# Kernel tuning notes

Measured on AMD Instinct MI355X. Metric: run time of the kernel, lower is better.

## Reference

```python
import jax, jax.numpy as jnp
import numpy as np
import math

B, S, D = 2, 2048, 2048
H = 16
DK = D // H


def build_rotary(dim, seq_len):
    inv_freq = 1.0 / (10000.0 ** (np.arange(0, dim, 2, dtype=np.float32) / dim))
    t = np.arange(seq_len, dtype=np.float32)
    freqs = np.einsum('i,j->ij', t, inv_freq)
    emb = np.concatenate([freqs, freqs], axis=-1)  # [S, dim]
    return jnp.asarray(np.cos(emb))[None, None], jnp.asarray(np.sin(emb))[None, None]


def rotate_half(x):
    x1, x2 = jnp.split(x, 2, axis=-1)
    return jnp.concatenate([-x2, x1], axis=-1)


def setup_inputs() -> dict:
    key = jax.random.key(0)
    ks = jax.random.split(key, 12)
    s = 1.0 / math.sqrt(D)
    inp = {
        'query': jax.random.normal(ks[0], (B, S, D), jnp.float32),
        'key': jax.random.normal(ks[1], (B, S, D), jnp.float32),
        'value': jax.random.normal(ks[2], (B, S, D), jnp.float32),
        'mask': jnp.tril(jnp.ones((S, S), bool))[None, None],  # causal [1,1,S,S]
        'wq': jax.random.uniform(ks[3], (D, D), jnp.float32, -s, s),
        'bq': jax.random.uniform(ks[4], (D,), jnp.float32, -s, s),
        'wk': jax.random.uniform(ks[5], (D, D), jnp.float32, -s, s),
        'bk': jax.random.uniform(ks[6], (D,), jnp.float32, -s, s),
        'wv': jax.random.uniform(ks[7], (D, D), jnp.float32, -s, s),
        'bv': jax.random.uniform(ks[8], (D,), jnp.float32, -s, s),
        'wo': jax.random.uniform(ks[9], (D, D), jnp.float32, -s, s),
        'bo': jax.random.uniform(ks[10], (D,), jnp.float32, -s, s),
    }
    return inp


def reference(query, key, value, mask, wq, bq, wk, bk, wv, bv, wo, bo):
    Bc, Sc, _ = query.shape
    # QKV projections -> [B, H, S, DK]
    def proj(x, w, b):
        return (x @ w.T + b).reshape(Bc, Sc, H, DK).transpose(0, 2, 1, 3)
    q = proj(query, wq, bq)
    k = proj(key, wk, bk)
    v = proj(value, wv, bv)
    # inline RoPE
    cos, sin = build_rotary(DK, Sc)
    cos = cos.astype(query.dtype)
    sin = sin.astype(query.dtype)
    q = q * cos + rotate_half(q) * sin
    k = k * cos + rotate_half(k) * sin
    # attention (dropout in eval / identity)
    scores = jnp.einsum('bhqd,bhkd->bhqk', q, k) / math.sqrt(DK)
    scores = jnp.where(mask, scores.astype(jnp.float32), -1e9)
    p = jax.nn.softmax(scores, axis=-1)
    x = jnp.einsum('bhqk,bhkd->bhqd', p, v)
    x = x.transpose(0, 2, 1, 3).reshape(Bc, Sc, H * DK)
    return x @ wo.T + bo
```

## Files before the change

### kernel.cpp

```cpp
#include <hip/hip_runtime.h>
#include <hip/hip_bf16.h>

#define Bc 2
#define Sc 2048
#define Dc 2048
#define Hc 16
#define DKc 128
#define Mc (Bc * Sc)
#define Kc Dc
#define Nc Dc
#define NX ((size_t)Bc * Sc * Dc)
#define NW ((size_t)Dc * Dc)

#define SM_C 0.1275174366f

typedef unsigned short u16;
using bf16x8  = __bf16 __attribute__((ext_vector_type(8)));
using ushort8 = unsigned short __attribute__((ext_vector_type(8)));
using ushort4v = unsigned short __attribute__((ext_vector_type(4)));
using floatx4 = float __attribute__((ext_vector_type(4)));
using float4v = float __attribute__((ext_vector_type(4)));

__device__ __forceinline__ u16 f2bf(float f) {
  union { float f; unsigned u; } x; x.f = f;
  unsigned r = x.u + 0x7fffu + ((x.u >> 16) & 1u);
  return (u16)(r >> 16);
}
__device__ __forceinline__ float bf2f(u16 u) {
  union { unsigned u; float f; } x; x.u = ((unsigned)u) << 16;
  return x.f;
}
__device__ __forceinline__ bf16x8 load8(const u16* p) {
  return __builtin_bit_cast(bf16x8, *(const ushort8*)p);
}
__device__ __forceinline__ floatx4 mfma16(bf16x8 a, bf16x8 b, floatx4 c) {
  return __builtin_amdgcn_mfma_f32_16x16x32_bf16(a, b, c, 0, 0, 0);
}
__device__ __forceinline__ void async16(const void* g, void* l) {
  __builtin_amdgcn_global_load_lds(
      (__attribute__((address_space(1))) void*)(g),
      (__attribute__((address_space(3))) void*)(l), 16, 0, 0);
}

__global__ __launch_bounds__(256) void cast_all(
    const float* __restrict__ q, const float* __restrict__ k,
    const float* __restrict__ v, const float* __restrict__ wq,
    const float* __restrict__ wk, const float* __restrict__ wv,
    const float* __restrict__ wo, u16* __restrict__ dst) {
  size_t i4 = (size_t)blockIdx.x * 256 + threadIdx.x;
  size_t e = i4 * 4;
  const float* src; size_t off;
  if (e < 3 * NX) {
    size_t w = e / NX;
    src = (w == 0) ? q : (w == 1) ? k : v;
    off = e - w * NX;
  } else {
    size_t e2 = e - 3 * NX;
    size_t w = e2 / NW;
    src = (w == 0) ? wq : (w == 1) ? wk : (w == 2) ? wv : wo;
    off = e2 - w * NW;
  }
  float4v val = *(const float4v*)(src + off);
  ushort4v o;
  o.x = f2bf(val.x); o.y = f2bf(val.y); o.z = f2bf(val.z); o.w = f2bf(val.w);
  *(ushort4v*)(dst + e) = o;
}

__device__ __forceinline__ void gemm_body(
    const u16* __restrict__ A, const u16* __restrict__ W,
    const float* __restrict__ bias, u16* __restrict__ out_bf,
    float* __restrict__ out_f, int epi, int m0, int n0, u16* Asl, u16* Bsl) {
  const int tid = threadIdx.x;
  const int wid = tid >> 6, lane = tid & 63;
  const int l15 = lane & 15, quad = lane >> 4;
  const int wm = wid & 1, wn = wid >> 1;

  floatx4 acc[4][4] = {};
  const int row_s = tid >> 2;
  const int col_s = (tid & 3) * 8;

  for (int k0 = 0; k0 < Kc; k0 += 32) {
    __syncthreads();
    const u16* ga0 = A + (size_t)(m0 + row_s) * Kc + k0 + col_s;
    const u16* gb0 = W + (size_t)(n0 + row_s) * Kc + k0 + col_s;
    async16(ga0, &Asl[tid * 8]);
    async16(ga0 + (size_t)64 * Kc, &Asl[2048 + tid * 8]);
    async16(gb0, &Bsl[tid * 8]);
    async16(gb0 + (size_t)64 * Kc, &Bsl[2048 + tid * 8]);
    __syncthreads();
    bf16x8 af[4], bfr[4];
#pragma unroll
    for (int i = 0; i < 4; i++)
      af[i] = load8(&Asl[(wm * 64 + i * 16 + l15) * 32 + quad * 8]);
#pragma unroll
    for (int j = 0; j < 4; j++)
      bfr[j] = load8(&Bsl[(wn * 64 + j * 16 + l15) * 32 + quad * 8]);
#pragma unroll
    for (int i = 0; i < 4; i++)
#pragma unroll
      for (int j = 0; j < 4; j++)
        acc[i][j] = mfma16(af[i], bfr[j], acc[i][j]);
  }

#pragma unroll
  for (int j = 0; j < 4; j++) {
    int col = n0 + wn * 64 + j * 16 + l15;
    float bv = bias[col];
#pragma unroll
    for (int i = 0; i < 4; i++) {
      int rowb = m0 + wm * 64 + i * 16 + quad * 4;
#pragma unroll
      for (int r = 0; r < 4; r++) {
        float v = acc[i][j][r] + bv;
        int row = rowb + r;
        if (epi == 2) {
          out_f[(size_t)row * Nc + col] = v;
        } else {
          int b = row >> 11, s = row & 2047;
          int h = col >> 7, dk = col & 127;
          size_t addr = (epi == 0)
              ? ((size_t)(b * Hc + h) * Sc + s) * DKc + dk
              : ((size_t)(b * Hc + h) * DKc + dk) * Sc + s;
          out_bf[addr] = f2bf(v);
        }
      }
    }
  }
}

__global__ __launch_bounds__(256, 2) void gemm_qkv(
    const u16* __restrict__ xq, const u16* __restrict__ xk,
    const u16* __restrict__ xv, const u16* __restrict__ wcat,
    const float* __restrict__ bq, const float* __restrict__ bk,
    const float* __restrict__ bv, u16* __restrict__ qhw,
    u16* __restrict__ khw, u16* __restrict__ vtw) {
  __shared__ u16 Asl[128 * 32];
  __shared__ u16 Bsl[128 * 32];
  const int proj = blockIdx.x >> 4;
  const int n0 = (blockIdx.x & 15) * 128;
  const int m0 = blockIdx.y * 128;
  const u16* A = (proj == 0) ? xq : (proj == 1) ? xk : xv;
  const u16* W = wcat + (size_t)proj * 2048 * Kc;
  const float* bias = (proj == 0) ? bq : (proj == 1) ? bk : bv;
  u16* outp = (proj == 0) ? qhw : (proj == 1) ? khw : vtw;
  gemm_body(A, W, bias, outp, nullptr, (proj == 2) ? 1 : 0, m0, n0, Asl, Bsl);
}

__global__ __launch_bounds__(256, 2) void gemm_out(
    const u16* __restrict__ A, const u16* __restrict__ W,
    const float* __restrict__ bias, float* __restrict__ out_f) {
  __shared__ u16 Asl[128 * 32];
  __shared__ u16 Bsl[128 * 32];
  gemm_body(A, W, bias, nullptr, out_f, 2, blockIdx.y * 128, blockIdx.x * 128,
            Asl, Bsl);
}

__global__ __launch_bounds__(256) void rope_kernel(u16* __restrict__ q,
                                                   u16* __restrict__ k) {
  int i = blockIdx.x * 256 + threadIdx.x;
  int d = i & 63;
  int s = (i >> 6) & (Sc - 1);
  int bh = i >> 17;
  size_t base = ((size_t)bh * Sc + s) * DKc;
  float inv_freq = exp2f((float)d * (-13.287712379549449f / 64.0f));
  float ang = (float)s * inv_freq;
  float sn, cs;
  sincosf(ang, &sn, &cs);
  float q1 = bf2f(q[base + d]), q2 = bf2f(q[base + d + 64]);
  q[base + d]      = f2bf((q1 * cs - q2 * sn) * SM_C);
  q[base + d + 64] = f2bf((q2 * cs + q1 * sn) * SM_C);
  float k1 = bf2f(k[base + d]), k2 = bf2f(k[base + d + 64]);
  k[base + d]      = f2bf(k1 * cs - k2 * sn);
  k[base + d + 64] = f2bf(k2 * cs + k1 * sn);
}

__global__ __launch_bounds__(256) void attn_kernel(
    const u16* __restrict__ qh, const u16* __restrict__ kh,
    const u16* __restrict__ vt, u16* __restrict__ ao) {
  __shared__ u16 Ksl[128 * 128];
  __shared__ u16 Vsl[144 * 128];
  const int tid = threadIdx.x;
  const int wid = tid >> 6, lane = tid & 63;
  const int l15 = lane & 15, quad = lane >> 4;
  const int qt = (blockIdx.z == 0) ? 15 - (int)blockIdx.x : (int)blockIdx.x;
  const int h = blockIdx.y, bb = blockIdx.z;
  const int bh = bb * Hc + h;
  const int q0 = qt * 128;
  const u16* qbase = qh + (size_t)bh * Sc * DKc;
  const u16* kbase = kh + (size_t)bh * Sc * DKc;
  const u16* vbase = vt + (size_t)bh * DKc * Sc;

  const int srow = tid >> 4;
  const int scol = (tid & 15) * 8;
  const int sdst = ((tid & 15) ^ srow) * 8;

  {
    int r = 128 + srow;
    u16 val = (r == 128) ? (u16)0x3F80 : (u16)0;
#pragma unroll
    for (int j = 0; j < 8; j++) Vsl[r * 128 + scol + j] = val;
  }

  bf16x8 qf[2][4];
#pragma unroll
  for (int mt = 0; mt < 2; mt++)
#pragma unroll
    for (int kq = 0; kq < 4; kq++)
      qf[mt][kq] = load8(qbase + (size_t)(q0 + wid * 32 + mt * 16 + l15) * DKc +
                         kq * 32 + quad * 8);

  floatx4 accO[2][9] = {};

  ushort8 kr[8], vr[8];
#pragma unroll
  for (int c = 0; c < 8; c++) {
    int rr = c * 16 + srow;
    kr[c] = *(const ushort8*)(kbase + (size_t)rr * DKc + scol);
    vr[c] = *(const ushort8*)(vbase + (size_t)rr * Sc + scol);
  }

  for (int kt = 0; kt <= qt; kt++) {
    __syncthreads();
#pragma unroll
    for (int c = 0; c < 8; c++) {
      int rr = c * 16 + srow;
      *(ushort8*)&Ksl[rr * 128 + sdst] = kr[c];
      *(ushort8*)&Vsl[rr * 128 + sdst] = vr[c];
    }
    __syncthreads();

    floatx4 sacc[2][8] = {};
#pragma unroll
    for (int kk = 0; kk < 4; kk++) {
      const int sb = ((kk * 4 + quad) ^ l15) * 8;
#pragma unroll
      for (int nt = 0; nt < 8; nt++) {
        bf16x8 kf = load8(&Ksl[(nt * 16 + l15) * 128 + sb]);
        sacc[0][nt] = mfma16(qf[0][kk], kf, sacc[0][nt]);
        sacc[1][nt] = mfma16(qf[1][kk], kf, sacc[1][nt]);
      }
    }

    if (kt == qt) {
#pragma unroll
      for (int nt = 0; nt < 8; nt++) {
        int kcol = nt * 16 + l15;
#pragma unroll
        for (int mt = 0; mt < 2; mt++) {
          int qrow = wid * 32 + mt * 16 + quad * 4;
#pragma unroll
          for (int r = 0; r < 4; r++)
            if (kcol > qrow + r) sacc[mt][nt][r] = -1e30f;
        }
      }
    }

#pragma unroll
    for (int mt = 0; mt < 2; mt++)
#pragma unroll
      for (int nt = 0; nt < 8; nt++)
#pragma unroll
        for (int r = 0; r < 4; r++)
          sacc[mt][nt][r] = exp2f(sacc[mt][nt][r]);

    __syncthreads();

    u16* Pw = &Ksl[wid * 4096];
#pragma unroll
    for (int mt = 0; mt < 2; mt++)
#pragma unroll
      for (int nt = 0; nt < 8; nt++)
#pragma unroll
        for (int r = 0; r < 4; r++) {
          int row = mt * 16 + quad * 4 + r;
          int col = nt * 16 + l15;
          int sb = (col >> 3) ^ (row & 15);
          Pw[row * 128 + sb * 8 + (col & 7)] = f2bf(sacc[mt][nt][r]);
        }

    if (kt < qt) {
      const u16* kb = kbase + (size_t)(kt + 1) * 128 * DKc;
#pragma unroll
      for (int c = 0; c < 8; c++) {
        int rr = c * 16 + srow;
        kr[c] = *(const ushort8*)(kb + (size_t)rr * DKc + scol);
        vr[c] = *(const ushort8*)(vbase + (size_t)rr * Sc + (kt + 1) * 128 + scol);
      }
    }

#pragma unroll
    for (int kk = 0; kk < 4; kk++) {
      const int sb = ((kk * 4 + quad) ^ l15) * 8;
      bf16x8 pf0 = load8(&Pw[(0 * 16 + l15) * 128 + sb]);
      bf16x8 pf1 = load8(&Pw[(1 * 16 + l15) * 128 + sb]);
#pragma unroll
      for (int nt = 0; nt < 9; nt++) {
        bf16x8 vf = load8(&Vsl[(nt * 16 + l15) * 128 + sb]);
        accO[0][nt] = mfma16(pf0, vf, accO[0][nt]);
        accO[1][nt] = mfma16(pf1, vf, accO[1][nt]);
      }
    }
  }

#pragma unroll
  for (int mt = 0; mt < 2; mt++)
#pragma unroll
    for (int r = 0; r < 4; r++) {
      float lsum = __shfl(accO[mt][8][r], lane & 48);
      float inv = 1.0f / lsum;
      int gq = q0 + wid * 32 + mt * 16 + quad * 4 + r;
      size_t rowbase = ((size_t)bb * Sc + gq) * Dc + h * DKc;
#pragma unroll
      for (int nt = 0; nt < 8; nt++)
        ao[rowbase + nt * 16 + l15] = f2bf(accO[mt][nt][r] * inv);
    }
}

extern "C" void kernel_launch(void* const* d_in, const int* in_sizes, int n_in,
                              void* d_out, int out_size, void* d_ws,
                              size_t ws_size, hipStream_t stream) {
  const float* q  = (const float*)d_in[0];
  const float* k  = (const float*)d_in[1];
  const float* v  = (const float*)d_in[2];
  const float* wq = (const float*)d_in[4];
  const float* bq = (const float*)d_in[5];
  const float* wk = (const float*)d_in[6];
  const float* bk = (const float*)d_in[7];
  const float* wv = (const float*)d_in[8];
  const float* bv = (const float*)d_in[9];
  const float* wo = (const float*)d_in[10];
  const float* bo = (const float*)d_in[11];
  float* out = (float*)d_out;

  u16* ws = (u16*)d_ws;
  u16* xq  = ws;
  u16* xk  = ws + NX;
  u16* xv  = ws + 2 * NX;
  u16* wcat = ws + 3 * NX;
  u16* wob = ws + 3 * NX + 3 * NW;
  u16* qhw = ws + 3 * NX + 4 * NW;
  u16* khw = ws + 4 * NX + 4 * NW;
  u16* vtw = ws + 5 * NX + 4 * NW;
  u16* aow = ws + 6 * NX + 4 * NW;

  {
    size_t tot4 = (3 * NX + 4 * NW) / 4;
    cast_all<<<dim3((unsigned)(tot4 / 256)), 256, 0, stream>>>(
        q, k, v, wq, wk, wv, wo, ws);
  }
  gemm_qkv<<<dim3(48, Mc / 128), 256, 0, stream>>>(
      xq, xk, xv, wcat, bq, bk, bv, qhw, khw, vtw);
  rope_kernel<<<dim3(Bc * Hc * Sc * 64 / 256), 256, 0, stream>>>(qhw, khw);
  attn_kernel<<<dim3(Sc / 128, Hc, Bc), 256, 0, stream>>>(qhw, khw, vtw, aow);
  gemm_out<<<dim3(Nc / 128, Mc / 128), 256, 0, stream>>>(aow, wob, bo, out);
}
```

Before: 534.3 us.

## Fuse Q RoPE into attention, skip masked diagonal tiles, raise GEMM occupancy

Q's rotary embedding and softmax scaling now run inside the attention kernel on register-held Q fragments, so the separate pass only rotates K. That removes one global read/write round trip over Q. On the diagonal tile, MFMAs and exp2 for fully masked 16-wide column blocks are skipped. The row-sum ones column is built in registers instead of extra LDS rows. GEMM launch bounds rise to 4 blocks per CU, which may force register spilling.

```diff
diff --git a/kernel.cpp b/kernel.cpp
--- a/kernel.cpp
+++ b/kernel.cpp
@@ -128,7 +128,7 @@
   }
 }
 
-__global__ __launch_bounds__(256, 2) void gemm_qkv(
+__global__ __launch_bounds__(256, 4) void gemm_qkv(
     const u16* __restrict__ xq, const u16* __restrict__ xk,
     const u16* __restrict__ xv, const u16* __restrict__ wcat,
     const float* __restrict__ bq, const float* __restrict__ bk,
@@ -146,7 +146,7 @@
   gemm_body(A, W, bias, outp, nullptr, (proj == 2) ? 1 : 0, m0, n0, Asl, Bsl);
 }
 
-__global__ __launch_bounds__(256, 2) void gemm_out(
+__global__ __launch_bounds__(256, 4) void gemm_out(
     const u16* __restrict__ A, const u16* __restrict__ W,
     const float* __restrict__ bias, float* __restrict__ out_f) {
   __shared__ u16 Asl[128 * 32];
@@ -155,8 +155,7 @@
             Asl, Bsl);
 }
 
-__global__ __launch_bounds__(256) void rope_kernel(u16* __restrict__ q,
-                                                   u16* __restrict__ k) {
+__global__ __launch_bounds__(256) void rope_k(u16* __restrict__ k) {
   int i = blockIdx.x * 256 + threadIdx.x;
   int d = i & 63;
   int s = (i >> 6) & (Sc - 1);
@@ -166,9 +165,6 @@
   float ang = (float)s * inv_freq;
   float sn, cs;
   sincosf(ang, &sn, &cs);
-  float q1 = bf2f(q[base + d]), q2 = bf2f(q[base + d + 64]);
-  q[base + d]      = f2bf((q1 * cs - q2 * sn) * SM_C);
-  q[base + d + 64] = f2bf((q2 * cs + q1 * sn) * SM_C);
   float k1 = bf2f(k[base + d]), k2 = bf2f(k[base + d + 64]);
   k[base + d]      = f2bf(k1 * cs - k2 * sn);
   k[base + d + 64] = f2bf(k2 * cs + k1 * sn);
@@ -178,7 +174,7 @@
     const u16* __restrict__ qh, const u16* __restrict__ kh,
     const u16* __restrict__ vt, u16* __restrict__ ao) {
   __shared__ u16 Ksl[128 * 128];
-  __shared__ u16 Vsl[144 * 128];
+  __shared__ u16 Vsl[128 * 128];
   const int tid = threadIdx.x;
   const int wid = tid >> 6, lane = tid & 63;
   const int l15 = lane & 15, quad = lane >> 4;
@@ -194,20 +190,46 @@
   const int scol = (tid & 15) * 8;
   const int sdst = ((tid & 15) ^ srow) * 8;
 
+  bf16x8 qf[2][4];
   {
-    int r = 128 + srow;
-    u16 val = (r == 128) ? (u16)0x3F80 : (u16)0;
-#pragma unroll
-    for (int j = 0; j < 8; j++) Vsl[r * 128 + scol + j] = val;
-  }
-
-  bf16x8 qf[2][4];
-#pragma unroll
-  for (int mt = 0; mt < 2; mt++)
-#pragma unroll
-    for (int kq = 0; kq < 4; kq++)
-      qf[mt][kq] = load8(qbase + (size_t)(q0 + wid * 32 + mt * 16 + l15) * DKc +
-                         kq * 32 + quad * 8);
+    ushort8 qr[2][4];
+#pragma unroll
+    for (int mt = 0; mt < 2; mt++)
+#pragma unroll
+      for (int kq = 0; kq < 4; kq++)
+        qr[mt][kq] = *(const ushort8*)(qbase +
+            (size_t)(q0 + wid * 32 + mt * 16 + l15) * DKc + kq * 32 + quad * 8);
+#pragma unroll
+    for (int kq = 0; kq < 2; kq++)
+#pragma unroll
+      for (int j = 0; j < 8; j++) {
+        int dd = kq * 32 + quad * 8 + j;
+        float inv_freq = exp2f((float)dd * (-13.287712379549449f / 64.0f));
+#pragma unroll
+        for (int mt = 0; mt < 2; mt++) {
+          float ang = (float)(q0 + wid * 32 + mt * 16 + l15) * inv_freq;
+          float sn, cs;
+          sincosf(ang, &sn, &cs);
+          float a = bf2f(qr[mt][kq][j]), b2 = bf2f(qr[mt][kq + 2][j]);
+          qr[mt][kq][j]     = f2bf((a * cs - b2 * sn) * SM_C);
+          qr[mt][kq + 2][j] = f2bf((b2 * cs + a * sn) * SM_C);
+        }
+      }
+#pragma unroll
+    for (int mt = 0; mt < 2; mt++)
+#pragma unroll
+      for (int kq = 0; kq < 4; kq++)
+        qf[mt][kq] = __builtin_bit_cast(bf16x8, qr[mt][kq]);
+  }
+
+  bf16x8 lfrag;
+  {
+    ushort8 lo = {};
+    if (l15 == 0)
+#pragma unroll
+      for (int j = 0; j < 8; j++) lo[j] = 0x3F80;
+    lfrag = __builtin_bit_cast(bf16x8, lo);
+  }
 
   floatx4 accO[2][9] = {};
 
@@ -230,38 +252,52 @@
     __syncthreads();
 
     floatx4 sacc[2][8] = {};
-#pragma unroll
-    for (int kk = 0; kk < 4; kk++) {
-      const int sb = ((kk * 4 + quad) ^ l15) * 8;
-#pragma unroll
-      for (int nt = 0; nt < 8; nt++) {
-        bf16x8 kf = load8(&Ksl[(nt * 16 + l15) * 128 + sb]);
-        sacc[0][nt] = mfma16(qf[0][kk], kf, sacc[0][nt]);
-        sacc[1][nt] = mfma16(qf[1][kk], kf, sacc[1][nt]);
-      }
-    }
-
-    if (kt == qt) {
-#pragma unroll
-      for (int nt = 0; nt < 8; nt++) {
-        int kcol = nt * 16 + l15;
-#pragma unroll
-        for (int mt = 0; mt < 2; mt++) {
-          int qrow = wid * 32 + mt * 16 + quad * 4;
+    if (kt < qt) {
+#pragma unroll
+      for (int kk = 0; kk < 4; kk++) {
+        const int sb = ((kk * 4 + quad) ^ l15) * 8;
+#pragma unroll
+        for (int nt = 0; nt < 8; nt++) {
+          bf16x8 kf = load8(&Ksl[(nt * 16 + l15) * 128 + sb]);
+          sacc[0][nt] = mfma16(qf[0][kk], kf, sacc[0][nt]);
+          sacc[1][nt] = mfma16(qf[1][kk], kf, sacc[1][nt]);
+        }
+      }
+#pragma unroll
+      for (int mt = 0; mt < 2; mt++)
+#pragma unroll
+        for (int nt = 0; nt < 8; nt++)
 #pragma unroll
           for (int r = 0; r < 4; r++)
-            if (kcol > qrow + r) sacc[mt][nt][r] = -1e30f;
-        }
-      }
-    }
-
-#pragma unroll
-    for (int mt = 0; mt < 2; mt++)
-#pragma unroll
-      for (int nt = 0; nt < 8; nt++)
-#pragma unroll
-        for (int r = 0; r < 4; r++)
-          sacc[mt][nt][r] = exp2f(sacc[mt][nt][r]);
+            sacc[mt][nt][r] = exp2f(sacc[mt][nt][r]);
+    } else {
+      const int lim0 = 2 * wid, lim1 = 2 * wid + 1;
+#pragma unroll
+      for (int kk = 0; kk < 4; kk++) {
+        const int sb = ((kk * 4 + quad) ^ l15) * 8;
+#pragma unroll
+        for (int nt = 0; nt < 8; nt++)
+          if (nt <= lim1) {
+            bf16x8 kf = load8(&Ksl[(nt * 16 + l15) * 128 + sb]);
+            if (nt <= lim0) sacc[0][nt] = mfma16(qf[0][kk], kf, sacc[0][nt]);
+            sacc[1][nt] = mfma16(qf[1][kk], kf, sacc[1][nt]);
+          }
+      }
+#pragma unroll
+      for (int r = 0; r < 4; r++)
+        if (l15 > quad * 4 + r) {
+          sacc[0][lim0][r] = -1e30f;
+          sacc[1][lim1][r] = -1e30f;
+        }
+#pragma unroll
+      for (int mt = 0; mt < 2; mt++)
+#pragma unroll
+        for (int nt = 0; nt < 8; nt++)
+          if (nt <= lim0 + mt)
+#pragma unroll
+            for (int r = 0; r < 4; r++)
+              sacc[mt][nt][r] = exp2f(sacc[mt][nt][r]);
+    }
 
     __syncthreads();
 
@@ -295,7 +331,7 @@
       bf16x8 pf1 = load8(&Pw[(1 * 16 + l15) * 128 + sb]);
 #pragma unroll
       for (int nt = 0; nt < 9; nt++) {
-        bf16x8 vf = load8(&Vsl[(nt * 16 + l15) * 128 + sb]);
+        bf16x8 vf = (nt < 8) ? load8(&Vsl[(nt * 16 + l15) * 128 + sb]) : lfrag;
         accO[0][nt] = mfma16(pf0, vf, accO[0][nt]);
         accO[1][nt] = mfma16(pf1, vf, accO[1][nt]);
       }
@@ -350,7 +386,7 @@
   }
   gemm_qkv<<<dim3(48, Mc / 128), 256, 0, stream>>>(
       xq, xk, xv, wcat, bq, bk, bv, qhw, khw, vtw);
-  rope_kernel<<<dim3(Bc * Hc * Sc * 64 / 256), 256, 0, stream>>>(qhw, khw);
+  rope_k<<<dim3(Bc * Hc * Sc * 64 / 256), 256, 0, stream>>>(khw);
   attn_kernel<<<dim3(Sc / 128, Hc, Bc), 256, 0, stream>>>(qhw, khw, vtw, aow);
   gemm_out<<<dim3(Nc / 128, Mc / 128), 256, 0, stream>>>(aow, wob, bo, out);
 }
```

New measurement: 687.2 us. 28.6% more time.
